# Kernel optimization log

Measured on AMD Instinct MI355X. Metric: run time of the kernel, lower is better.

The kernel has to match this reference:

```python
import jax, jax.numpy as jnp
import numpy as np

N = 50000      # nodes
E = 400000     # edges
IN = 128       # in_channels
HID = 64       # hidden_channels (per head)
H = 4          # heads
OUT = 10       # classes
G = 64         # graphs in batch


def setup_inputs() -> dict:
    key = jax.random.key(0)
    ks = jax.random.split(key, 32)
    s = 0.05
    inp = {
        "x": jax.random.normal(ks[0], (N, IN), dtype=jnp.float32),
        "edge_index": jax.random.randint(ks[1], (2, E), 0, N, dtype=jnp.int32),
        "batch": jnp.sort(jax.random.randint(ks[2], (N,), 0, G, dtype=jnp.int32)),
    }
    # TransformerConv layer 1 params (in=IN -> heads*HID)
    d1 = H * HID
    inp["Wq1"] = jax.random.normal(ks[3], (IN, d1)) * s
    inp["bq1"] = jnp.zeros((d1,), jnp.float32)
    inp["Wk1"] = jax.random.normal(ks[4], (IN, d1)) * s
    inp["bk1"] = jnp.zeros((d1,), jnp.float32)
    inp["Wv1"] = jax.random.normal(ks[5], (IN, d1)) * s
    inp["bv1"] = jnp.zeros((d1,), jnp.float32)
    inp["Ws1"] = jax.random.normal(ks[6], (IN, d1)) * s   # root/skip weight
    inp["bs1"] = jnp.zeros((d1,), jnp.float32)
    # TransformerConv layer 2 params (in=H*HID -> heads*HID)
    inp["Wq2"] = jax.random.normal(ks[7], (d1, d1)) * s
    inp["bq2"] = jnp.zeros((d1,), jnp.float32)
    inp["Wk2"] = jax.random.normal(ks[8], (d1, d1)) * s
    inp["bk2"] = jnp.zeros((d1,), jnp.float32)
    inp["Wv2"] = jax.random.normal(ks[9], (d1, d1)) * s
    inp["bv2"] = jnp.zeros((d1,), jnp.float32)
    inp["Ws2"] = jax.random.normal(ks[10], (d1, d1)) * s
    inp["bs2"] = jnp.zeros((d1,), jnp.float32)
    # final classifier
    inp["Wl"] = jax.random.normal(ks[11], (d1, OUT)) * s
    inp["bl"] = jnp.zeros((OUT,), jnp.float32)
    return inp


def transformer_conv(x, src, dst, Wq, bq, Wk, bk, Wv, bv, Ws, bs):
    """PyG TransformerConv (concat=True, root_weight=True, beta=None, eval mode).
    src = edge_index[0] (source j), dst = edge_index[1] (target i).
    """
    n = x.shape[0]
    q = (x @ Wq + bq).reshape(n, H, HID)
    k = (x @ Wk + bk).reshape(n, H, HID)
    v = (x @ Wv + bv).reshape(n, H, HID)
    # per-edge attention logits [E, H]
    alpha = jnp.einsum('ehc,ehc->eh', q[dst], k[src]) / np.sqrt(HID).astype(np.float32)
    # scatter-softmax over incoming edges of each target node
    amax = jax.ops.segment_max(alpha, dst, num_segments=n)           # [N, H], -inf for isolated
    ex = jnp.exp(alpha - amax[dst])                                   # [E, H]
    denom = jax.ops.segment_sum(ex, dst, num_segments=n) + 1e-16      # [N, H]
    w = ex / denom[dst]                                               # normalized alpha [E, H]
    # scatter-sum aggregation of weighted values
    out = jax.ops.segment_sum(w[:, :, None] * v[src], dst, num_segments=n)  # [N, H, HID]
    out = out.reshape(n, H * HID)
    return out + (x @ Ws + bs)  # root/skip connection


def reference(x, edge_index, batch,
              Wq1, bq1, Wk1, bk1, Wv1, bv1, Ws1, bs1,
              Wq2, bq2, Wk2, bk2, Wv2, bv2, Ws2, bs2,
              Wl, bl):
    src, dst = edge_index[0], edge_index[1]
    h = jax.nn.elu(transformer_conv(x, src, dst, Wq1, bq1, Wk1, bk1, Wv1, bv1, Ws1, bs1))
    h = jax.nn.elu(transformer_conv(h, src, dst, Wq2, bq2, Wk2, bk2, Wv2, bv2, Ws2, bs2))
    # global mean pool per graph
    sums = jax.ops.segment_sum(h, batch, num_segments=G)              # [G, H*HID]
    cnt = jax.ops.segment_sum(jnp.ones((h.shape[0],), h.dtype), batch, num_segments=G)
    pooled = sums / jnp.maximum(cnt, 1.0)[:, None]
    logits = pooled @ Wl + bl
    return jax.nn.log_softmax(logits, axis=-1)
```

## Files before the change

### kernel.cpp

```cpp
#include <hip/hip_runtime.h>
#include <math.h>

constexpr int NN   = 50000;
constexpr int NE   = 400000;
constexpr int INC  = 128;
constexpr int NH   = 4;
constexpr int D1   = 256;
constexpr int D4   = 1024;
constexpr int NOUT = 10;
constexpr int NG   = 64;
constexpr int NB_SCAN = (NN + 255) / 256;


typedef __attribute__((ext_vector_type(8))) short bf16x8;
typedef __attribute__((ext_vector_type(4))) float f32x4;
typedef __attribute__((ext_vector_type(2))) float f32x2;

__device__ __forceinline__ short f2b(float f) {
  union { float f; unsigned int i; } v; v.f = f;
  unsigned int x = v.i;
  return (short)((x + 0x7FFFu + ((x >> 16) & 1u)) >> 16);
}
__device__ __forceinline__ float b2f(short u) {
  union { unsigned int i; float f; } v; v.i = ((unsigned int)(unsigned short)u) << 16;
  return v.f;
}
__device__ __forceinline__ float4 ld4b(const short* p) {
  short4 u = *(const short4*)p;
  return make_float4(b2f(u.x), b2f(u.y), b2f(u.z), b2f(u.w));
}
__device__ __forceinline__ int pk_fp8x4(float a, float b, float c, float d) {
  int v = __builtin_amdgcn_cvt_pk_fp8_f32(a, b, 0, false);
  v = __builtin_amdgcn_cvt_pk_fp8_f32(c, d, v, true);
  return v;
}

__device__ __forceinline__ void gld_lds16(const short* g, short* l) {
  __builtin_amdgcn_global_load_lds(
      (const __attribute__((address_space(1))) unsigned int*)g,
      (__attribute__((address_space(3))) unsigned int*)l, 16, 0, 0);
}

constexpr int CVT_XB  = (NN * INC / 4 + 255) / 256;
constexpr int CVT_W1B = (4 * D1 * INC + 255) / 256;
constexpr int CVT_W2B = (4 * D1 * D1 + 255) / 256;
constexpr int CVT_BB  = 8;
constexpr int CVT_DB  = (NN + 255) / 256;
constexpr int CVT_SB  = (NG * D1 + 255) / 256;

__device__ __forceinline__ void wt_one(const float* Wq, const float* Wk,
    const float* Wv, const float* Ws, short* Wt, int kbits, int i) {
  int K = 1 << kbits;
  int seg = i >> (kbits + 8);
  int idx = i & ((D1 << kbits) - 1);
  int n = idx >> kbits, k = idx & (K - 1);
  const float* W = (seg == 0) ? Wq : (seg == 1) ? Wk : (seg == 2) ? Wv : Ws;
  int row;
  if (seg == 0)      row = n;
  else if (seg == 3) row = 768 + n;
  else               row = 256 + (n >> 2) * 8 + ((seg == 2) ? 4 : 0) + (n & 3);
  Wt[(size_t)row * K + k] = f2b(W[(size_t)k * D1 + n]);
}

__global__ void cvt_all_k(const float* __restrict__ x, short* __restrict__ Xb,
    const float* __restrict__ Wq1, const float* __restrict__ Wk1,
    const float* __restrict__ Wv1, const float* __restrict__ Ws1,
    const float* __restrict__ Wq2, const float* __restrict__ Wk2,
    const float* __restrict__ Wv2, const float* __restrict__ Ws2,
    short* __restrict__ Wtc1, short* __restrict__ Wtc2,
    const float* __restrict__ bq1, const float* __restrict__ bk1,
    const float* __restrict__ bv1, const float* __restrict__ bs1,
    const float* __restrict__ bq2, const float* __restrict__ bk2,
    const float* __restrict__ bv2, const float* __restrict__ bs2,
    float* __restrict__ bc1, float* __restrict__ bc2,
    int* __restrict__ deg, float* __restrict__ sums) {
  const int b = blockIdx.x;
  const int t = threadIdx.x;
  if (b < CVT_XB) {
    int i = (b * 256 + t) * 4;
    if (i >= NN * INC) return;
    float4 v = *(const float4*)(x + i);
    short4 o; o.x = f2b(v.x); o.y = f2b(v.y); o.z = f2b(v.z); o.w = f2b(v.w);
    *(short4*)(Xb + i) = o;
  } else if (b < CVT_XB + CVT_W1B) {
    int i = (b - CVT_XB) * 256 + t;
    if (i < 4 * D1 * INC) wt_one(Wq1, Wk1, Wv1, Ws1, Wtc1, 7, i);
  } else if (b < CVT_XB + CVT_W1B + CVT_W2B) {
    int i = (b - CVT_XB - CVT_W1B) * 256 + t;
    if (i < 4 * D1 * D1) wt_one(Wq2, Wk2, Wv2, Ws2, Wtc2, 8, i);
  } else if (b < CVT_XB + CVT_W1B + CVT_W2B + CVT_BB) {
    int i = (b - CVT_XB - CVT_W1B - CVT_W2B) * 256 + t;
    if (i >= 2 * D4) return;
    int row = i & (D4 - 1);
    const float* bq = (i < D4) ? bq1 : bq2;
    const float* bk = (i < D4) ? bk1 : bk2;
    const float* bv = (i < D4) ? bv1 : bv2;
    const float* bs = (i < D4) ? bs1 : bs2;
    float v;
    if (row < 256) v = bq[row];
    else if (row < 768) {
      int j = row - 256, grp = j >> 3, off = j & 7;
      int ch = grp * 4 + (off & 3);
      v = (off < 4) ? bk[ch] : bv[ch];
    } else v = bs[row - 768];
    ((i < D4) ? bc1 : bc2)[row] = v;
  } else if (b < CVT_XB + CVT_W1B + CVT_W2B + CVT_BB + CVT_DB) {
    int i = (b - CVT_XB - CVT_W1B - CVT_W2B - CVT_BB) * 256 + t;
    if (i < NN) deg[i] = 0;
  } else {
    int i = (b - CVT_XB - CVT_W1B - CVT_W2B - CVT_BB - CVT_DB) * 256 + t;
    if (i < NG * D1) sums[i] = 0.f;
  }
}

__global__ void deg_count(const int* __restrict__ dst, int* __restrict__ deg) {
  int e = blockIdx.x * 256 + threadIdx.x;
  if (e < NE) atomicAdd(&deg[dst[e]], 1);
}
__global__ __launch_bounds__(256) void scan1(const int* __restrict__ deg,
    int* __restrict__ partial, const int* __restrict__ batch, int* __restrict__ gb) {
  if (blockIdx.x == NB_SCAN) {
    int g = threadIdx.x;
    if (g > NG) return;
    int lo = 0, hi = NN;
    while (lo < hi) {
      int mid = (lo + hi) >> 1;
      if (batch[mid] < g) lo = mid + 1; else hi = mid;
    }
    gb[g] = lo;
    return;
  }
  __shared__ int sh[256];
  int t = threadIdx.x, i = blockIdx.x * 256 + t;
  sh[t] = (i < NN) ? deg[i] : 0;
  __syncthreads();
  for (int off = 128; off > 0; off >>= 1) {
    if (t < off) sh[t] += sh[t + off];
    __syncthreads();
  }
  if (t == 0) partial[blockIdx.x] = sh[0];
}
__global__ __launch_bounds__(256) void scan3(const int* __restrict__ deg,
    const int* __restrict__ partial, int* __restrict__ rowstart,
    int* __restrict__ cursor) {
  __shared__ int sh[256];
  __shared__ int base_s;
  const int t = threadIdx.x;
  int pv = (t < NB_SCAN) ? partial[t] : 0;
  sh[t] = pv;
  __syncthreads();
  for (int off = 1; off < 256; off <<= 1) {
    int o = (t >= off) ? sh[t - off] : 0;
    __syncthreads();
    sh[t] += o;
    __syncthreads();
  }
  if (t == 0) base_s = (blockIdx.x == 0) ? 0 : sh[blockIdx.x - 1];
  __syncthreads();
  const int base = base_s;
  __syncthreads();
  int i = blockIdx.x * 256 + t;
  int v = (i < NN) ? deg[i] : 0;
  sh[t] = v;
  __syncthreads();
  for (int off = 1; off < 256; off <<= 1) {
    int o = (t >= off) ? sh[t - off] : 0;
    __syncthreads();
    sh[t] += o;
    __syncthreads();
  }
  int excl = sh[t] - v + base;
  if (i <= NN) rowstart[i] = excl;
  if (i < NN)  cursor[i]   = excl;
}
__global__ void scatter_k(const int* __restrict__ src, const int* __restrict__ dst,
    int* __restrict__ cursor, int* __restrict__ esrc) {
  int e = blockIdx.x * 256 + threadIdx.x;
  if (e >= NE) return;
  int d = dst[e];
  int pos = atomicAdd(&cursor[d], 1);
  esrc[pos] = src[e];
}

__global__ __launch_bounds__(256) void gemm_mfma(
    const short* __restrict__ Xb, const short* __restrict__ Wt,
    const float* __restrict__ bias, short* __restrict__ QS,
    unsigned char* __restrict__ KV8, int M, int K) {
  __shared__ short smem[4 * 4096];
  short* As0 = smem;
  short* As1 = smem + 4096;
  short* Bs0 = smem + 8192;
  short* Bs1 = smem + 12288;
  const int bx = blockIdx.x;
  const int by = blockIdx.y;
  const int m_tile = (bx & 7) + (by << 3);
  const int n_tile = bx >> 3;
  const int m0 = m_tile * 128;
  if (m0 >= M) return;
  const int n0 = n_tile * 128;

  const int t    = threadIdx.x;
  const int lane = t & 63;
  const int wv   = t >> 6;
  const int wm   = (wv >> 1) * 64;
  const int wn   = (wv & 1) * 64;
  const int quad = lane >> 4;
  const int l16  = lane & 15;
  const int lrow = lane >> 2;
  const int lseg = lane & 3;

  const int swz_w = (lseg ^ ((lrow >> 1) & 3)) * 8;
  const int swz_r = (quad ^ ((l16 >> 1) & 3)) * 8;

  f32x4 acc[4][4] = {};
  for (int k0 = 0; k0 < K; k0 += 64) {
#pragma unroll
    for (int j = 0; j < 2; ++j) {
      const int rb = wv * 32 + j * 16;
      int gm = m0 + rb + lrow;
      gm = gm < M ? gm : M - 1;
      const size_t ga = (size_t)gm * K + k0 + swz_w;
      gld_lds16(Xb + ga,      &As0[rb * 32]);
      gld_lds16(Xb + ga + 32, &As1[rb * 32]);
      const size_t gw = (size_t)(n0 + rb + lrow) * K + k0 + swz_w;
      gld_lds16(Wt + gw,      &Bs0[rb * 32]);
      gld_lds16(Wt + gw + 32, &Bs1[rb * 32]);
    }
    __syncthreads();
    {
      bf16x8 a[4], b[4];
#pragma unroll
      for (int mi = 0; mi < 4; mi++)
        a[mi] = *(const bf16x8*)(&As0[(wm + mi * 16 + l16) * 32 + swz_r]);
#pragma unroll
      for (int nj = 0; nj < 4; nj++)
        b[nj] = *(const bf16x8*)(&Bs0[(wn + nj * 16 + l16) * 32 + swz_r]);
#pragma unroll
      for (int mi = 0; mi < 4; mi++)
#pragma unroll
        for (int nj = 0; nj < 4; nj++)
          acc[mi][nj] = __builtin_amdgcn_mfma_f32_16x16x32_bf16(b[nj], a[mi], acc[mi][nj], 0, 0, 0);
#pragma unroll
      for (int mi = 0; mi < 4; mi++)
        a[mi] = *(const bf16x8*)(&As1[(wm + mi * 16 + l16) * 32 + swz_r]);
#pragma unroll
      for (int nj = 0; nj < 4; nj++)
        b[nj] = *(const bf16x8*)(&Bs1[(wn + nj * 16 + l16) * 32 + swz_r]);
#pragma unroll
      for (int mi = 0; mi < 4; mi++)
#pragma unroll
        for (int nj = 0; nj < 4; nj++)
          acc[mi][nj] = __builtin_amdgcn_mfma_f32_16x16x32_bf16(b[nj], a[mi], acc[mi][nj], 0, 0, 0);
    }
    __syncthreads();
  }
  const bool isKV = (n_tile >= 2) && (n_tile <= 5);
  float4 bz[4];
#pragma unroll
  for (int nj = 0; nj < 4; nj++)
    bz[nj] = *(const float4*)(bias + n0 + wn + nj * 16 + quad * 4);
#pragma unroll
  for (int mi = 0; mi < 4; mi++) {
    const int m = m0 + wm + mi * 16 + l16;
    if (m >= M) continue;
#pragma unroll
    for (int nj = 0; nj < 4; nj++) {
      const int col = n0 + wn + nj * 16 + quad * 4;
      const float v0 = acc[mi][nj][0] + bz[nj].x;
      const float v1 = acc[mi][nj][1] + bz[nj].y;
      const float v2 = acc[mi][nj][2] + bz[nj].z;
      const float v3 = acc[mi][nj][3] + bz[nj].w;
      if (isKV) {
        const int p = pk_fp8x4(v0, v1, v2, v3);
        *(int*)(KV8 + (size_t)m * 512 + (col - 256)) = p;
      } else {
        short4 o;
        o.x = f2b(v0); o.y = f2b(v1); o.z = f2b(v2); o.w = f2b(v3);
        const int qc = (n_tile < 2) ? col : (col - 512);
        *(short4*)(QS + (size_t)m * 512 + qc) = o;
      }
    }
  }
}

__device__ __forceinline__ void dec_kv(const int2 x, float* k, float* v) {
  f32x2 a = __builtin_amdgcn_cvt_pk_f32_fp8(x.x, false);
  f32x2 b = __builtin_amdgcn_cvt_pk_f32_fp8(x.x, true);
  f32x2 c = __builtin_amdgcn_cvt_pk_f32_fp8(x.y, false);
  f32x2 d = __builtin_amdgcn_cvt_pk_f32_fp8(x.y, true);
  k[0] = a.x; k[1] = a.y; k[2] = b.x; k[3] = b.y;
  v[0] = c.x; v[1] = c.y; v[2] = d.x; v[3] = d.y;
}

template <typename TOUT>
__device__ __forceinline__ void st1(TOUT* p, float v);
template <> __device__ __forceinline__ void st1<float>(float* p, float v) { *p = v; }
template <> __device__ __forceinline__ void st1<short>(short* p, float v) { *p = f2b(v); }

template <typename TOUT>
__global__ __launch_bounds__(256) void node_attn(
    const int* __restrict__ rowstart, const int* __restrict__ esrc,
    const short* __restrict__ QS, const unsigned char* __restrict__ KV8,
    TOUT* __restrict__ out) {
  const int nid = blockIdx.x * 4 + (threadIdx.x >> 6);
  if (nid >= NN) return;
  const int t  = threadIdx.x & 63;
  const int c0 = t * 4;
  const int r0 = __builtin_amdgcn_readfirstlane(rowstart[nid]);
  const int r1 = __builtin_amdgcn_readfirstlane(rowstart[nid + 1]);
  const float4 q = ld4b(QS + (size_t)nid * 512 + c0);
  const unsigned char* kvb = KV8 + t * 8;
  float m = -INFINITY, denom = 0.f;
  float4 acc = make_float4(0.f, 0.f, 0.f, 0.f);
  int r = r0;
  for (; r + 7 < r1; r += 8) {
    const int e0 = __builtin_amdgcn_readfirstlane(esrc[r + 0]);
    const int e1 = __builtin_amdgcn_readfirstlane(esrc[r + 1]);
    const int e2 = __builtin_amdgcn_readfirstlane(esrc[r + 2]);
    const int e3 = __builtin_amdgcn_readfirstlane(esrc[r + 3]);
    const int e4 = __builtin_amdgcn_readfirstlane(esrc[r + 4]);
    const int e5 = __builtin_amdgcn_readfirstlane(esrc[r + 5]);
    const int e6 = __builtin_amdgcn_readfirstlane(esrc[r + 6]);
    const int e7 = __builtin_amdgcn_readfirstlane(esrc[r + 7]);
    const int2 x0 = *(const int2*)(kvb + (size_t)e0 * 512);
    const int2 x1 = *(const int2*)(kvb + (size_t)e1 * 512);
    const int2 x2 = *(const int2*)(kvb + (size_t)e2 * 512);
    const int2 x3 = *(const int2*)(kvb + (size_t)e3 * 512);
    const int2 x4 = *(const int2*)(kvb + (size_t)e4 * 512);
    const int2 x5 = *(const int2*)(kvb + (size_t)e5 * 512);
    const int2 x6 = *(const int2*)(kvb + (size_t)e6 * 512);
    const int2 x7 = *(const int2*)(kvb + (size_t)e7 * 512);
    float k0[4], v0[4], k1[4], v1[4], k2[4], v2[4], k3[4], v3[4];
    float k4[4], v4[4], k5[4], v5[4], k6[4], v6[4], k7[4], v7[4];
    dec_kv(x0, k0, v0); dec_kv(x1, k1, v1);
    dec_kv(x2, k2, v2); dec_kv(x3, k3, v3);
    dec_kv(x4, k4, v4); dec_kv(x5, k5, v5);
    dec_kv(x6, k6, v6); dec_kv(x7, k7, v7);
    float d0 = q.x * k0[0] + q.y * k0[1] + q.z * k0[2] + q.w * k0[3];
    float d1 = q.x * k1[0] + q.y * k1[1] + q.z * k1[2] + q.w * k1[3];
    float d2 = q.x * k2[0] + q.y * k2[1] + q.z * k2[2] + q.w * k2[3];
    float d3 = q.x * k3[0] + q.y * k3[1] + q.z * k3[2] + q.w * k3[3];
    float d4 = q.x * k4[0] + q.y * k4[1] + q.z * k4[2] + q.w * k4[3];
    float d5 = q.x * k5[0] + q.y * k5[1] + q.z * k5[2] + q.w * k5[3];
    float d6 = q.x * k6[0] + q.y * k6[1] + q.z * k6[2] + q.w * k6[3];
    float d7 = q.x * k7[0] + q.y * k7[1] + q.z * k7[2] + q.w * k7[3];
#pragma unroll
    for (int off = 1; off <= 8; off <<= 1) {
      d0 += __shfl_xor(d0, off, 16);
      d1 += __shfl_xor(d1, off, 16);
      d2 += __shfl_xor(d2, off, 16);
      d3 += __shfl_xor(d3, off, 16);
      d4 += __shfl_xor(d4, off, 16);
      d5 += __shfl_xor(d5, off, 16);
      d6 += __shfl_xor(d6, off, 16);
      d7 += __shfl_xor(d7, off, 16);
    }
    d0 *= 0.125f; d1 *= 0.125f; d2 *= 0.125f; d3 *= 0.125f;
    d4 *= 0.125f; d5 *= 0.125f; d6 *= 0.125f; d7 *= 0.125f;
    const float t01 = fmaxf(d0, d1), t23 = fmaxf(d2, d3);
    const float t45 = fmaxf(d4, d5), t67 = fmaxf(d6, d7);
    const float nm = fmaxf(fmaxf(m, fmaxf(t01, t23)), fmaxf(t45, t67));
    const float sc  = __expf(m - nm);
    const float ex0 = __expf(d0 - nm);
    const float ex1 = __expf(d1 - nm);
    const float ex2 = __expf(d2 - nm);
    const float ex3 = __expf(d3 - nm);
    const float ex4 = __expf(d4 - nm);
    const float ex5 = __expf(d5 - nm);
    const float ex6 = __expf(d6 - nm);
    const float ex7 = __expf(d7 - nm);
    denom = denom * sc + ((ex0 + ex1) + (ex2 + ex3)) + ((ex4 + ex5) + (ex6 + ex7));
    acc.x = acc.x * sc + ex0 * v0[0] + ex1 * v1[0] + ex2 * v2[0] + ex3 * v3[0]
                       + ex4 * v4[0] + ex5 * v5[0] + ex6 * v6[0] + ex7 * v7[0];
    acc.y = acc.y * sc + ex0 * v0[1] + ex1 * v1[1] + ex2 * v2[1] + ex3 * v3[1]
                       + ex4 * v4[1] + ex5 * v5[1] + ex6 * v6[1] + ex7 * v7[1];
    acc.z = acc.z * sc + ex0 * v0[2] + ex1 * v1[2] + ex2 * v2[2] + ex3 * v3[2]
                       + ex4 * v4[2] + ex5 * v5[2] + ex6 * v6[2] + ex7 * v7[2];
    acc.w = acc.w * sc + ex0 * v0[3] + ex1 * v1[3] + ex2 * v2[3] + ex3 * v3[3]
                       + ex4 * v4[3] + ex5 * v5[3] + ex6 * v6[3] + ex7 * v7[3];
    m = nm;
  }
  for (; r + 3 < r1; r += 4) {
    const int e0 = __builtin_amdgcn_readfirstlane(esrc[r + 0]);
    const int e1 = __builtin_amdgcn_readfirstlane(esrc[r + 1]);
    const int e2 = __builtin_amdgcn_readfirstlane(esrc[r + 2]);
    const int e3 = __builtin_amdgcn_readfirstlane(esrc[r + 3]);
    const int2 x0 = *(const int2*)(kvb + (size_t)e0 * 512);
    const int2 x1 = *(const int2*)(kvb + (size_t)e1 * 512);
    const int2 x2 = *(const int2*)(kvb + (size_t)e2 * 512);
    const int2 x3 = *(const int2*)(kvb + (size_t)e3 * 512);
    float k0[4], v0[4], k1[4], v1[4], k2[4], v2[4], k3[4], v3[4];
    dec_kv(x0, k0, v0); dec_kv(x1, k1, v1);
    dec_kv(x2, k2, v2); dec_kv(x3, k3, v3);
    float d0 = q.x * k0[0] + q.y * k0[1] + q.z * k0[2] + q.w * k0[3];
    float d1 = q.x * k1[0] + q.y * k1[1] + q.z * k1[2] + q.w * k1[3];
    float d2 = q.x * k2[0] + q.y * k2[1] + q.z * k2[2] + q.w * k2[3];
    float d3 = q.x * k3[0] + q.y * k3[1] + q.z * k3[2] + q.w * k3[3];
#pragma unroll
    for (int off = 1; off <= 8; off <<= 1) {
      d0 += __shfl_xor(d0, off, 16);
      d1 += __shfl_xor(d1, off, 16);
      d2 += __shfl_xor(d2, off, 16);
      d3 += __shfl_xor(d3, off, 16);
    }
    d0 *= 0.125f; d1 *= 0.125f; d2 *= 0.125f; d3 *= 0.125f;
    const float nm = fmaxf(fmaxf(m, fmaxf(d0, d1)), fmaxf(d2, d3));
    const float sc = __expf(m - nm);
    const float ex0 = __expf(d0 - nm);
    const float ex1 = __expf(d1 - nm);
    const float ex2 = __expf(d2 - nm);
    const float ex3 = __expf(d3 - nm);
    denom = denom * sc + ex0 + ex1 + ex2 + ex3;
    acc.x = acc.x * sc + ex0 * v0[0] + ex1 * v1[0] + ex2 * v2[0] + ex3 * v3[0];
    acc.y = acc.y * sc + ex0 * v0[1] + ex1 * v1[1] + ex2 * v2[1] + ex3 * v3[1];
    acc.z = acc.z * sc + ex0 * v0[2] + ex1 * v1[2] + ex2 * v2[2] + ex3 * v3[2];
    acc.w = acc.w * sc + ex0 * v0[3] + ex1 * v1[3] + ex2 * v2[3] + ex3 * v3[3];
    m = nm;
  }
  for (; r < r1; r++) {
    const int e0 = __builtin_amdgcn_readfirstlane(esrc[r]);
    const int2 x0 = *(const int2*)(kvb + (size_t)e0 * 512);
    float k0[4], v0[4];
    dec_kv(x0, k0, v0);
    float d0 = q.x * k0[0] + q.y * k0[1] + q.z * k0[2] + q.w * k0[3];
#pragma unroll
    for (int off = 1; off <= 8; off <<= 1) d0 += __shfl_xor(d0, off, 16);
    d0 *= 0.125f;
    const float nm = fmaxf(m, d0);
    const float sc = __expf(m - nm);
    const float ex0 = __expf(d0 - nm);
    denom = denom * sc + ex0;
    acc.x = acc.x * sc + ex0 * v0[0];
    acc.y = acc.y * sc + ex0 * v0[1];
    acc.z = acc.z * sc + ex0 * v0[2];
    acc.w = acc.w * sc + ex0 * v0[3];
    m = nm;
  }
  const float inv = 1.0f / (denom + 1e-16f);
  const float4 sk = ld4b(QS + (size_t)nid * 512 + 256 + c0);
  float o0 = acc.x * inv + sk.x;
  float o1 = acc.y * inv + sk.y;
  float o2 = acc.z * inv + sk.z;
  float o3 = acc.w * inv + sk.w;
  o0 = o0 > 0.f ? o0 : expm1f(o0);
  o1 = o1 > 0.f ? o1 : expm1f(o1);
  o2 = o2 > 0.f ? o2 : expm1f(o2);
  o3 = o3 > 0.f ? o3 : expm1f(o3);
  TOUT* p = out + (size_t)nid * D1 + c0;
  st1<TOUT>(p + 0, o0); st1<TOUT>(p + 1, o1);
  st1<TOUT>(p + 2, o2); st1<TOUT>(p + 3, o3);
}

__global__ __launch_bounds__(256) void pool_k(const float* __restrict__ h,
    const int* __restrict__ batch, float* __restrict__ sums) {
  const int c = threadIdx.x;
  const int n0 = blockIdx.x * 64;
  const int n1 = min(n0 + 64, NN);
  float run = 0.f;
  int curg = -1;
  for (int n = n0; n < n1; n++) {
    int g = batch[n];
    if (g != curg) {
      if (curg >= 0) atomicAdd(&sums[(size_t)curg * D1 + c], run);
      run = 0.f; curg = g;
    }
    run += h[(size_t)n * D1 + c];
  }
  if (curg >= 0) atomicAdd(&sums[(size_t)curg * D1 + c], run);
}

__global__ __launch_bounds__(640) void head_k(const float* __restrict__ sums,
    const int* __restrict__ gb, const float* __restrict__ Wl,
    const float* __restrict__ bl, float* __restrict__ out) {
  __shared__ float logits[NG][NOUT];
  const int t = threadIdx.x;
  if (t < NG * NOUT) {
    int g = t / NOUT, o = t % NOUT;
    float inv = 1.0f / fmaxf((float)(gb[g + 1] - gb[g]), 1.0f);
    float acc = 0.f;
    for (int k = 0; k < D1; k++) acc += sums[(size_t)g * D1 + k] * Wl[k * NOUT + o];
    logits[g][o] = acc * inv + bl[o];
  }
  __syncthreads();
  if (t < NG) {
    float mx = -INFINITY;
#pragma unroll
    for (int o = 0; o < NOUT; o++) mx = fmaxf(mx, logits[t][o]);
    float s = 0.f;
#pragma unroll
    for (int o = 0; o < NOUT; o++) s += __expf(logits[t][o] - mx);
    float lse = mx + logf(s);
#pragma unroll
    for (int o = 0; o < NOUT; o++) out[t * NOUT + o] = logits[t][o] - lse;
  }
}

extern "C" void kernel_launch(void* const* d_in, const int* in_sizes, int n_in,
                              void* d_out, int out_size, void* d_ws, size_t ws_size,
                              hipStream_t stream) {
  const float* x   = (const float*)d_in[0];
  const int* ei    = (const int*)d_in[1];
  const int* batch = (const int*)d_in[2];
  const float* Wq1 = (const float*)d_in[3];  const float* bq1 = (const float*)d_in[4];
  const float* Wk1 = (const float*)d_in[5];  const float* bk1 = (const float*)d_in[6];
  const float* Wv1 = (const float*)d_in[7];  const float* bv1 = (const float*)d_in[8];
  const float* Ws1 = (const float*)d_in[9];  const float* bs1 = (const float*)d_in[10];
  const float* Wq2 = (const float*)d_in[11]; const float* bq2 = (const float*)d_in[12];
  const float* Wk2 = (const float*)d_in[13]; const float* bk2 = (const float*)d_in[14];
  const float* Wv2 = (const float*)d_in[15]; const float* bv2 = (const float*)d_in[16];
  const float* Ws2 = (const float*)d_in[17]; const float* bs2 = (const float*)d_in[18];
  const float* Wl  = (const float*)d_in[19]; const float* bl  = (const float*)d_in[20];

  const int* srcIdx = ei;
  const int* dstIdx = ei + NE;

  float* ws = (float*)d_ws;
  const size_t SZ_NODE = (size_t)NN * D1;
  float* H2f  = ws;
  float* sums = ws + SZ_NODE;
  float* bc1  = sums + (size_t)NG * D1;
  float* bc2  = bc1 + D4;
  short* Xb   = (short*)(bc2 + D4);
  short* H1b  = Xb + (size_t)NN * INC;
  short* QS   = H1b + SZ_NODE;
  short* Wtc1 = QS + (size_t)NN * 512;
  short* Wtc2 = Wtc1 + (size_t)D4 * INC;
  unsigned char* KV8 = (unsigned char*)(Wtc2 + (size_t)D4 * D1);
  int* ip      = (int*)(KV8 + (size_t)NN * 512);
  int* deg     = ip;
  int* partial = deg + NN;
  int* rowstart= partial + 256;
  int* cursor  = rowstart + NN + 1;
  int* esrc    = cursor + NN;
  int* gb      = esrc + NE;

  const int mtiles = (NN + 127) / 128;
  const dim3 gemmGrid(64, (mtiles + 7) / 8);
  const int edgeBlocks = (NE + 255) / 256;
  const int aggBlocks  = (NN + 3) / 4;
  const int cvtBlocks  = CVT_XB + CVT_W1B + CVT_W2B + CVT_BB + CVT_DB + CVT_SB;

  cvt_all_k<<<cvtBlocks, 256, 0, stream>>>(x, Xb,
      Wq1, Wk1, Wv1, Ws1, Wq2, Wk2, Wv2, Ws2, Wtc1, Wtc2,
      bq1, bk1, bv1, bs1, bq2, bk2, bv2, bs2, bc1, bc2, deg, sums);

  deg_count<<<edgeBlocks, 256, 0, stream>>>(dstIdx, deg);
  scan1<<<NB_SCAN + 1, 256, 0, stream>>>(deg, partial, batch, gb);
  scan3<<<NB_SCAN, 256, 0, stream>>>(deg, partial, rowstart, cursor);
  scatter_k<<<edgeBlocks, 256, 0, stream>>>(srcIdx, dstIdx, cursor, esrc);

  gemm_mfma<<<gemmGrid, 256, 0, stream>>>(Xb, Wtc1, bc1, QS, KV8, NN, INC);
  node_attn<short><<<aggBlocks, 256, 0, stream>>>(rowstart, esrc, QS, KV8, H1b);

  gemm_mfma<<<gemmGrid, 256, 0, stream>>>(H1b, Wtc2, bc2, QS, KV8, NN, D1);
  node_attn<float><<<aggBlocks, 256, 0, stream>>>(rowstart, esrc, QS, KV8, H2f);

  pool_k<<<(NN + 63) / 64, 256, 0, stream>>>(H2f, batch, sums);
  head_k<<<1, 640, 0, stream>>>(sums, gb, Wl, bl, (float*)d_out);
}
```

Before: 398.1 us.

## Double-buffer GEMM K-loop and stage epilogue through LDS for coalesced stores

```diff
diff --git a/kernel.cpp b/kernel.cpp
--- a/kernel.cpp
+++ b/kernel.cpp
@@ -182,15 +182,13 @@
   esrc[pos] = src[e];
 }
 
+constexpr int CLDS = 136;
+
 __global__ __launch_bounds__(256) void gemm_mfma(
     const short* __restrict__ Xb, const short* __restrict__ Wt,
     const float* __restrict__ bias, short* __restrict__ QS,
     unsigned char* __restrict__ KV8, int M, int K) {
-  __shared__ short smem[4 * 4096];
-  short* As0 = smem;
-  short* As1 = smem + 4096;
-  short* Bs0 = smem + 8192;
-  short* Bs1 = smem + 12288;
+  __shared__ short smem[128 * CLDS];
   const int bx = blockIdx.x;
   const int by = blockIdx.y;
   const int m_tile = (bx & 7) + (by << 3);
@@ -213,72 +211,109 @@
   const int swz_r = (quad ^ ((l16 >> 1) & 3)) * 8;
 
   f32x4 acc[4][4] = {};
-  for (int k0 = 0; k0 < K; k0 += 64) {
+
+  {
 #pragma unroll
     for (int j = 0; j < 2; ++j) {
-      const int rb = wv * 32 + j * 16;
+      const int rb = (wv * 2 + j) * 16;
       int gm = m0 + rb + lrow;
       gm = gm < M ? gm : M - 1;
-      const size_t ga = (size_t)gm * K + k0 + swz_w;
-      gld_lds16(Xb + ga,      &As0[rb * 32]);
-      gld_lds16(Xb + ga + 32, &As1[rb * 32]);
-      const size_t gw = (size_t)(n0 + rb + lrow) * K + k0 + swz_w;
-      gld_lds16(Wt + gw,      &Bs0[rb * 32]);
-      gld_lds16(Wt + gw + 32, &Bs1[rb * 32]);
-    }
-    __syncthreads();
+      gld_lds16(Xb + (size_t)gm * K + swz_w,              &smem[rb * 32]);
+      gld_lds16(Wt + (size_t)(n0 + rb + lrow) * K + swz_w, &smem[4096 + rb * 32]);
+    }
+  }
+  __syncthreads();
+
+  int cur = 0;
+  for (int k0 = 0; k0 < K; k0 += 32) {
+    if (k0 + 32 < K) {
+      short* An = &smem[(cur ^ 1) * 8192];
+      short* Bn = &smem[(cur ^ 1) * 8192 + 4096];
+#pragma unroll
+      for (int j = 0; j < 2; ++j) {
+        const int rb = (wv * 2 + j) * 16;
+        int gm = m0 + rb + lrow;
+        gm = gm < M ? gm : M - 1;
+        gld_lds16(Xb + (size_t)gm * K + k0 + 32 + swz_w,              &An[rb * 32]);
+        gld_lds16(Wt + (size_t)(n0 + rb + lrow) * K + k0 + 32 + swz_w, &Bn[rb * 32]);
+      }
+    }
     {
+      const short* Ac = &smem[cur * 8192];
+      const short* Bc = &smem[cur * 8192 + 4096];
       bf16x8 a[4], b[4];
 #pragma unroll
       for (int mi = 0; mi < 4; mi++)
-        a[mi] = *(const bf16x8*)(&As0[(wm + mi * 16 + l16) * 32 + swz_r]);
+        a[mi] = *(const bf16x8*)(&Ac[(wm + mi * 16 + l16) * 32 + swz_r]);
 #pragma unroll
       for (int nj = 0; nj < 4; nj++)
-        b[nj] = *(const bf16x8*)(&Bs0[(wn + nj * 16 + l16) * 32 + swz_r]);
+        b[nj] = *(const bf16x8*)(&Bc[(wn + nj * 16 + l16) * 32 + swz_r]);
 #pragma unroll
       for (int mi = 0; mi < 4; mi++)
 #pragma unroll
         for (int nj = 0; nj < 4; nj++)
           acc[mi][nj] = __builtin_amdgcn_mfma_f32_16x16x32_bf16(b[nj], a[mi], acc[mi][nj], 0, 0, 0);
-#pragma unroll
-      for (int mi = 0; mi < 4; mi++)
-        a[mi] = *(const bf16x8*)(&As1[(wm + mi * 16 + l16) * 32 + swz_r]);
-#pragma unroll
-      for (int nj = 0; nj < 4; nj++)
-        b[nj] = *(const bf16x8*)(&Bs1[(wn + nj * 16 + l16) * 32 + swz_r]);
-#pragma unroll
-      for (int mi = 0; mi < 4; mi++)
-#pragma unroll
-        for (int nj = 0; nj < 4; nj++)
-          acc[mi][nj] = __builtin_amdgcn_mfma_f32_16x16x32_bf16(b[nj], a[mi], acc[mi][nj], 0, 0, 0);
-    }
-    __syncthreads();
-  }
+    }
+    __syncthreads();
+    cur ^= 1;
+  }
+
   const bool isKV = (n_tile >= 2) && (n_tile <= 5);
   float4 bz[4];
 #pragma unroll
   for (int nj = 0; nj < 4; nj++)
     bz[nj] = *(const float4*)(bias + n0 + wn + nj * 16 + quad * 4);
-#pragma unroll
-  for (int mi = 0; mi < 4; mi++) {
-    const int m = m0 + wm + mi * 16 + l16;
-    if (m >= M) continue;
-#pragma unroll
-    for (int nj = 0; nj < 4; nj++) {
-      const int col = n0 + wn + nj * 16 + quad * 4;
-      const float v0 = acc[mi][nj][0] + bz[nj].x;
-      const float v1 = acc[mi][nj][1] + bz[nj].y;
-      const float v2 = acc[mi][nj][2] + bz[nj].z;
-      const float v3 = acc[mi][nj][3] + bz[nj].w;
-      if (isKV) {
-        const int p = pk_fp8x4(v0, v1, v2, v3);
-        *(int*)(KV8 + (size_t)m * 512 + (col - 256)) = p;
-      } else {
+
+  if (isKV) {
+    unsigned char* cs = (unsigned char*)smem;
+#pragma unroll
+    for (int mi = 0; mi < 4; mi++) {
+      const int row = wm + mi * 16 + l16;
+#pragma unroll
+      for (int nj = 0; nj < 4; nj++) {
+        const int colb = wn + nj * 16 + quad * 4;
+        const int p = pk_fp8x4(acc[mi][nj][0] + bz[nj].x, acc[mi][nj][1] + bz[nj].y,
+                               acc[mi][nj][2] + bz[nj].z, acc[mi][nj][3] + bz[nj].w);
+        *(int*)(cs + row * 136 + colb) = p;
+      }
+    }
+    __syncthreads();
+    const int kv_base = n0 - 256;
+#pragma unroll
+    for (int it = 0; it < 8; ++it) {
+      const int chunk = it * 256 + t;
+      const int row = chunk >> 4;
+      const int cb  = (chunk & 15) * 8;
+      const int gm  = m0 + row;
+      if (gm >= M) continue;
+      *(int2*)(KV8 + (size_t)gm * 512 + kv_base + cb) = *(const int2*)(cs + row * 136 + cb);
+    }
+  } else {
+#pragma unroll
+    for (int mi = 0; mi < 4; mi++) {
+      const int row = wm + mi * 16 + l16;
+#pragma unroll
+      for (int nj = 0; nj < 4; nj++) {
+        const int col = wn + nj * 16 + quad * 4;
         short4 o;
-        o.x = f2b(v0); o.y = f2b(v1); o.z = f2b(v2); o.w = f2b(v3);
-        const int qc = (n_tile < 2) ? col : (col - 512);
-        *(short4*)(QS + (size_t)m * 512 + qc) = o;
+        o.x = f2b(acc[mi][nj][0] + bz[nj].x);
+        o.y = f2b(acc[mi][nj][1] + bz[nj].y);
+        o.z = f2b(acc[mi][nj][2] + bz[nj].z);
+        o.w = f2b(acc[mi][nj][3] + bz[nj].w);
+        *(short4*)(&smem[row * CLDS + col]) = o;
       }
+    }
+    __syncthreads();
+    const int qs_base = (n_tile < 2) ? n0 : (n0 - 512);
+#pragma unroll
+    for (int it = 0; it < 8; ++it) {
+      const int chunk = it * 256 + t;
+      const int row = chunk >> 4;
+      const int cc  = (chunk & 15) * 8;
+      const int gm  = m0 + row;
+      if (gm >= M) continue;
+      const int4 s4 = *(const int4*)(&smem[row * CLDS + cc]);
+      *(int4*)(QS + (size_t)gm * 512 + qs_base + cc) = s4;
     }
   }
 }
```

Measured after the change: 363.8 us. -8.6%, faster.
